# Kernel optimization log

Measured on AMD Instinct MI355X. Metric: run time of the kernel, lower is better.

The kernel has to match this reference:

```python
import jax, jax.numpy as jnp
import numpy as np

B, S, D, H, DK, DFF, L = 4, 1024, 1024, 16, 64, 4096, 128

def setup_inputs() -> dict:
    key = jax.random.key(0)
    ks = jax.random.split(key, 20)
    stdv = 1.0 / np.sqrt(D)
    u = lambda k, shape, s=stdv: jax.random.uniform(k, shape, jnp.float32, -s, s)
    x = jax.random.normal(ks[0], (B, S, D), jnp.float32)
    causal = jnp.triu(jnp.ones((S, S), bool), 1)          # True = masked
    attn_mask = jnp.broadcast_to(causal, (B, S, S))
    return {
        "x": x,
        "attn_mask": attn_mask,
        "W_q": u(ks[1], (H * DK, D)), "b_q": jnp.zeros((H * DK,)),
        "W_k": u(ks[2], (H * DK, D)), "b_k": jnp.zeros((H * DK,)),
        "W_v": u(ks[3], (H * DK, D)), "b_v": jnp.zeros((H * DK,)),
        "W_o": u(ks[4], (D, H * DK)), "b_o": jnp.zeros((D,)),
        "W_rel": u(ks[5], (2 * L + 1, DK), 1.0 / np.sqrt(DK)),
        "ln1_alpha": jnp.ones((D,)), "ln1_bias": jnp.zeros((D,)),
        "ln2_alpha": jnp.ones((D,)), "ln2_bias": jnp.zeros((D,)),
        "W1": u(ks[6], (DFF, D)), "b1": jnp.zeros((DFF,)),
        "W2": u(ks[7], (D, DFF)), "b2": jnp.zeros((D,)),
    }

def _layer_norm(x, alpha, bias, eps=1e-5):
    # Faithful to source: (x - mean) / (std + eps), std is biased (unbiased=False)
    m = jnp.mean(x, axis=-1, keepdims=True)
    std = jnp.sqrt(jnp.mean((x - m) ** 2, axis=-1, keepdims=True))
    return alpha * (x - m) / (std + eps) + bias

def reference(x, attn_mask, W_q, b_q, W_k, b_k, W_v, b_v, W_o, b_o, W_rel,
              ln1_alpha, ln1_bias, ln2_alpha, ln2_bias, W1, b1, W2, b2):
    b, s, d = x.shape
    q = (x @ W_q.T + b_q).reshape(b, s, H, DK)
    k = (x @ W_k.T + b_k).reshape(b, s, H, DK)
    v = (x @ W_v.T + b_v).reshape(b, s, H, DK)
    # relative position bias table lookup -> [s, s, DK]
    idx = jnp.clip(jnp.arange(s)[:, None] - jnp.arange(s)[None, :], -L, L) + L
    pos = W_rel[idx]
    # NOTE: original uses rel_pos_k_emb for BOTH pos_key and pos_value (as in source).
    scores = jnp.einsum('bqnd,bknd->bnqk', q, k) + jnp.einsum('bqnd,qkd->bnqk', q, pos)
    scores = scores / np.sqrt(DK)
    scores = jnp.where(attn_mask[:, None, :, :], jnp.float32(-10000.0), scores)
    attn = jax.nn.softmax(scores, axis=-1)
    out = jnp.einsum('bnqk,bknd->bnqd', attn, v) + jnp.einsum('bnqk,qkd->bnqd', attn, pos)
    out = out.transpose(0, 2, 1, 3).reshape(b, s, H * DK)
    out = out @ W_o.T + b_o
    # post-LN transformer layer: LN(x + attn), then LN(h + FFN(h))
    h = _layer_norm(x + out, ln1_alpha, ln1_bias)
    f = jax.nn.relu(h @ W1.T + b1) @ W2.T + b2
    return _layer_norm(h + f, ln2_alpha, ln2_bias)
```

## Files before the change

kernel.cpp:

```cpp
#include <hip/hip_runtime.h>
#include <cmath>
#include <cstdint>

typedef __bf16 bf16;
typedef __bf16 bf16x8 __attribute__((ext_vector_type(8)));
typedef __bf16 bf16x4 __attribute__((ext_vector_type(4)));
typedef float f32x4 __attribute__((ext_vector_type(4)));

#define CEXP 0.1803368852f

__device__ __forceinline__ void async_ld16(const void* g, void* l) {
  __builtin_amdgcn_global_load_lds(
      (__attribute__((address_space(1))) void*)(uintptr_t)g,
      (__attribute__((address_space(3))) void*)l, 16, 0, 0);
}

__global__ __launch_bounds__(256) void cast_all(
    const float* __restrict__ x,  const float* __restrict__ wq, const float* __restrict__ wk,
    const float* __restrict__ wv, const float* __restrict__ wo, const float* __restrict__ w1,
    const float* __restrict__ w2,
    bf16* xb, bf16* wqb, bf16* wkb, bf16* wvb, bf16* wob, bf16* w1b, bf16* w2b)
{
  int i = blockIdx.x * 256 + threadIdx.x;
  const int M1 = 1 << 20, Q = 1 << 18;
  const float* src; bf16* dst; int off;
  if      (i < M1)            { src = x;  dst = xb;  off = i; }
  else if (i < M1 + Q)        { src = wq; dst = wqb; off = i - M1; }
  else if (i < M1 + 2 * Q)    { src = wk; dst = wkb; off = i - M1 - Q; }
  else if (i < M1 + 3 * Q)    { src = wv; dst = wvb; off = i - M1 - 2 * Q; }
  else if (i < M1 + 4 * Q)    { src = wo; dst = wob; off = i - M1 - 3 * Q; }
  else if (i < 3 * M1)        { src = w1; dst = w1b; off = i - M1 - 4 * Q; }
  else                        { src = w2; dst = w2b; off = i - 3 * M1; }
  float4 v = ((const float4*)src)[off];
  bf16x4 o; o[0]=(bf16)v.x; o[1]=(bf16)v.y; o[2]=(bf16)v.z; o[3]=(bf16)v.w;
  ((bf16x4*)dst)[off] = o;
}

template<int BM>
__device__ __forceinline__ void gemm_core(
    const bf16* __restrict__ A, const bf16* __restrict__ Bm, const float* __restrict__ bias,
    float* __restrict__ outF, bf16* __restrict__ outB,
    const float* __restrict__ residF, const bf16* __restrict__ residB,
    int N, int kld, int kbeg, int kend, int relu, bf16* As, bf16* Bs)
{
  constexpr int MI = BM / 32;
  const int tid  = threadIdx.x;
  const int wave = tid >> 6, lane = tid & 63;
  const int lr = lane & 15, lq = lane >> 4;
  const int bm = blockIdx.x * BM, bn = blockIdx.y * 128;
  const int wm = (wave >> 1) * (BM / 2), wn = (wave & 1) * 64;
  const int srow = lane >> 2, scol = (lane & 3) * 8;

  const f32x4 fz = {0.f, 0.f, 0.f, 0.f};
  f32x4 acc[MI][4];
#pragma unroll
  for (int i = 0; i < MI; i++)
#pragma unroll
    for (int j = 0; j < 4; j++) acc[i][j] = fz;

  auto issue = [&](int k0, int buf) {
    bf16* Ad = As + buf * (BM * 32);
    bf16* Bd = Bs + buf * (128 * 32);
    if (BM == 128) {
#pragma unroll
      for (int cc = 0; cc < 2; ++cc) {
        int c = wave * 2 + cc;
        async_ld16(A + (size_t)(bm + c * 16 + srow) * kld + k0 + scol, Ad + c * 512);
      }
    } else {
      async_ld16(A + (size_t)(bm + wave * 16 + srow) * kld + k0 + scol, Ad + wave * 512);
    }
#pragma unroll
    for (int cc = 0; cc < 2; ++cc) {
      int c = wave * 2 + cc;
      async_ld16(Bm + (size_t)(bn + c * 16 + srow) * kld + k0 + scol, Bd + c * 512);
    }
  };

  const int nit = (kend - kbeg) >> 5;
  issue(kbeg, 0);
  for (int i = 0; i < nit; i++) {
    __syncthreads();
    if (i + 1 < nit) issue(kbeg + (i + 1) * 32, (i + 1) & 1);
    const bf16* Ab = As + (i & 1) * (BM * 32);
    const bf16* Bb = Bs + (i & 1) * (128 * 32);
    bf16x8 af[MI], bfr[4];
#pragma unroll
    for (int mi = 0; mi < MI; mi++) af[mi]  = *(const bf16x8*)(Ab + (wm + mi*16 + lr)*32 + lq*8);
#pragma unroll
    for (int ni = 0; ni < 4; ni++) bfr[ni] = *(const bf16x8*)(Bb + (wn + ni*16 + lr)*32 + lq*8);
#pragma unroll
    for (int mi = 0; mi < MI; mi++)
#pragma unroll
      for (int ni = 0; ni < 4; ni++)
        acc[mi][ni] = __builtin_amdgcn_mfma_f32_16x16x32_bf16(af[mi], bfr[ni], acc[mi][ni], 0, 0, 0);
  }

#pragma unroll
  for (int ni = 0; ni < 4; ni++) {
    int n = bn + wn + ni*16 + lr;
    float bv = bias ? bias[n] : 0.0f;
#pragma unroll
    for (int mi = 0; mi < MI; mi++) {
#pragma unroll
      for (int r = 0; r < 4; r++) {
        int m = bm + wm + mi*16 + lq*4 + r;
        size_t idx = (size_t)m * N + n;
        float v = acc[mi][ni][r] + bv;
        if (relu) v = fmaxf(v, 0.0f);
        if (residF) v += residF[idx];
        if (residB) v += (float)residB[idx];
        if (outF) outF[idx] = v;
        else      outB[idx] = (bf16)v;
      }
    }
  }
}

template<int BM>
__global__ __launch_bounds__(256) void gemm_bt(
    const bf16* A, const bf16* Bm, const float* bias,
    float* outF, bf16* outB, const float* residF, const bf16* residB,
    int N, int K, int relu)
{
  __shared__ bf16 As[2 * BM * 32];
  __shared__ bf16 Bs[2 * 128 * 32];
  gemm_core<BM>(A, Bm, bias, outF, outB, residF, residB, N, K, 0, K, relu, As, Bs);
}

__global__ __launch_bounds__(256) void gemm_splitk(
    const bf16* A, const bf16* Bm, float* part, int N, int kld, int kchunk)
{
  __shared__ bf16 As[2 * 128 * 32];
  __shared__ bf16 Bs[2 * 128 * 32];
  const int z = blockIdx.z;
  gemm_core<128>(A, Bm, nullptr, part + (size_t)z * 4096 * N, nullptr, nullptr, nullptr,
                 N, kld, z * kchunk, (z + 1) * kchunk, 0, As, Bs);
}

__global__ __launch_bounds__(256) void gemm_qkv(
    const bf16* A, const bf16* Bq, const bf16* Bk, const bf16* Bv,
    const float* bq, const float* bk, const float* bv,
    bf16* Oq, bf16* Ok, bf16* Ov, int N, int K)
{
  __shared__ bf16 As[2 * 128 * 32];
  __shared__ bf16 Bs[2 * 128 * 32];
  const bf16* Bm  = blockIdx.z == 0 ? Bq : (blockIdx.z == 1 ? Bk : Bv);
  const float* bi = blockIdx.z == 0 ? bq : (blockIdx.z == 1 ? bk : bv);
  bf16* O         = blockIdx.z == 0 ? Oq : (blockIdx.z == 1 ? Ok : Ov);
  gemm_core<128>(A, Bm, bi, nullptr, O, nullptr, nullptr, N, K, 0, K, 0, As, Bs);
}

__global__ __launch_bounds__(256) void transpose_v(const bf16* __restrict__ V, bf16* __restrict__ Vt) {
  __shared__ bf16 t[64][72];
  const int tid = threadIdx.x;
  const int sblk = blockIdx.x;
  const int bh = blockIdx.y;
  const int b = bh >> 4, h = bh & 15;
  const int sr = tid >> 2, dc = (tid & 3) * 16;
  const bf16* src = V + ((size_t)(b * 1024 + sblk * 64 + sr)) * 1024 + h * 64 + dc;
  bf16x8 r0 = *(const bf16x8*)src;
  bf16x8 r1 = *(const bf16x8*)(src + 8);
  *(bf16x8*)(&t[sr][dc]) = r0;
  *(bf16x8*)(&t[sr][dc + 8]) = r1;
  __syncthreads();
  const int dr = tid >> 2, sc = (tid & 3) * 16;
  bf16 o[16];
#pragma unroll
  for (int j = 0; j < 16; j++) o[j] = t[sc + j][dr];
  bf16* dst = Vt + ((size_t)(bh * 64 + dr)) * 1024 + sblk * 64 + sc;
  *(bf16x8*)dst = *(bf16x8*)&o[0];
  *(bf16x8*)(dst + 8) = *(bf16x8*)&o[8];
}

#define S_LEN 1024
#define ROWSTR 1024

__global__ __launch_bounds__(256) void attn_kernel(
    const bf16* __restrict__ Qg, const bf16* __restrict__ Kg, const bf16* __restrict__ Vt,
    const float* __restrict__ Wrel, bf16* __restrict__ Og)
{
  __shared__ __align__(16) bf16 hist[64][136];
  __shared__ __align__(16) bf16 rel_s[64][132];
  __shared__ __align__(16) bf16 ovl[8704];
  bf16* V_T  = ovl;
  bf16* Pb   = ovl + 4096;
  bf16* Wst  = ovl;
  bf16* Wr_t = ovl;
  float* lbuf = (float*)rel_s;
  float* hbuf = lbuf + 256;

  const int tid = threadIdx.x;
  const int wave = tid >> 6, lane = tid & 63;
  const int lr = lane & 15, lq = lane >> 4;
  const int qblk = 15 - blockIdx.x;
  const int bh = blockIdx.y;
  const int b = bh >> 4, h = bh & 15;
  const int q0 = qblk * 64;
  const int T = qblk + 1;
  const int nearStart = (T > 3) ? T - 3 : 0;
  const size_t rowbase = (size_t)b * S_LEN * ROWSTR + h * 64;
  const size_t vtbase = (size_t)(bh * 64) * 1024;
  const f32x4 fz = {0.f, 0.f, 0.f, 0.f};

  for (int e = tid; e < 128 * 64; e += 256)
    Wst[e] = (bf16)Wrel[(size_t)(128 + (e >> 6)) * 64 + (e & 63)];
  for (int e = tid; e < 64 * 68; e += 256) ((uint*)hist)[e] = 0u;

  bf16x8 qf[4][2];
#pragma unroll
  for (int qt = 0; qt < 4; qt++)
#pragma unroll
    for (int c = 0; c < 2; c++)
      qf[qt][c] = *(const bf16x8*)(Qg + rowbase + (size_t)(q0 + qt*16 + lr) * ROWSTR + c*32 + lq*8);

  bf16x8 wb[2];
#pragma unroll
  for (int c = 0; c < 2; c++)
#pragma unroll
    for (int j = 0; j < 8; j++)
      wb[c][j] = (bf16)Wrel[(size_t)256 * 64 + c*32 + lq*8 + j];

  __syncthreads();

#pragma unroll
  for (int tt = 0; tt < 2; ++tt)
#pragma unroll
    for (int qt = 0; qt < 4; ++qt) {
      f32x4 a = fz;
#pragma unroll
      for (int c = 0; c < 2; c++) {
        bf16x8 wf = *(const bf16x8*)(Wst + (wave*32 + tt*16 + lr) * 64 + c*32 + lq*8);
        a = __builtin_amdgcn_mfma_f32_16x16x32_bf16(wf, qf[qt][c], a, 0, 0, 0);
      }
      bf16x4 pk; pk[0]=(bf16)(a[0]*CEXP); pk[1]=(bf16)(a[1]*CEXP);
                 pk[2]=(bf16)(a[2]*CEXP); pk[3]=(bf16)(a[3]*CEXP);
      *(bf16x4*)(&rel_s[qt*16 + lr][wave*32 + tt*16 + lq*4]) = pk;
    }
  {
    f32x4 a = fz;
#pragma unroll
    for (int c = 0; c < 2; c++)
      a = __builtin_amdgcn_mfma_f32_16x16x32_bf16(wb[c], qf[wave][c], a, 0, 0, 0);
    if (lq == 0) rel_s[wave*16 + lr][128] = (bf16)(a[0]*CEXP);
  }
  __syncthreads();

  float relc[4];
#pragma unroll
  for (int qt = 0; qt < 4; qt++) relc[qt] = (float)rel_s[qt*16 + lr][128];

  float l_p[4] = {0.f,0.f,0.f,0.f}, h_p[4] = {0.f,0.f,0.f,0.f};
  f32x4 acc_o[4];
#pragma unroll
  for (int dt = 0; dt < 4; dt++) acc_o[dt] = fz;

  const int vd1 = tid >> 3;
  const int vj  = (tid & 7) ^ (vd1 & 7);
  const int krow = 16 * wave + lr;

  uint4 va, vb, va2, vb2;
  bf16x8 kf0, kf1, kn0, kn1;
  {
    const bf16* vp = Vt + vtbase + (size_t)vd1 * 1024 + vj * 8;
    va = *(const uint4*)vp; vb = *(const uint4*)(vp + 32 * 1024);
    const bf16* kp = Kg + rowbase + (size_t)krow * ROWSTR + lq*8;
    kf0 = *(const bf16x8*)kp; kf1 = *(const bf16x8*)(kp + 32);
  }

  for (int kt = 0; kt < T; ++kt) {
    const int k0 = kt * 64;

    f32x4 sc[4];
#pragma unroll
    for (int qt = 0; qt < 4; qt++) {
      sc[qt] = __builtin_amdgcn_mfma_f32_16x16x32_bf16(kf0, qf[qt][0], fz, 0, 0, 0);
      sc[qt] = __builtin_amdgcn_mfma_f32_16x16x32_bf16(kf1, qf[qt][1], sc[qt], 0, 0, 0);
    }
    if (kt + 1 < T) {
      const bf16* vp = Vt + vtbase + (size_t)vd1 * 1024 + k0 + 64 + vj * 8;
      va2 = *(const uint4*)vp; vb2 = *(const uint4*)(vp + 32 * 1024);
      const bf16* kp = Kg + rowbase + (size_t)(k0 + 64 + krow) * ROWSTR + lq*8;
      kn0 = *(const bf16x8*)kp; kn1 = *(const bf16x8*)(kp + 32);
    }

    float pw[4][4];
    if (kt < nearStart) {
#pragma unroll
      for (int qt = 0; qt < 4; qt++) {
#pragma unroll
        for (int r = 0; r < 4; r++) pw[qt][r] = exp2f(fmaf(sc[qt][r], CEXP, relc[qt]));
        float s4 = pw[qt][0] + pw[qt][1] + pw[qt][2] + pw[qt][3];
        l_p[qt] += s4; h_p[qt] += s4;
      }
    } else {
#pragma unroll
      for (int qt = 0; qt < 4; qt++) {
        int qg = q0 + qt*16 + lr;
#pragma unroll
        for (int r = 0; r < 4; r++) {
          int kg = k0 + 16*wave + lq*4 + r;
          float p = 0.0f;
          if (kg <= qg) {
            int t = qg - kg; int tc = t > 128 ? 128 : t;
            p = exp2f(fmaf(sc[qt][r], CEXP, (float)rel_s[qt*16 + lr][tc]));
            l_p[qt] += p;
            if (t >= 128) h_p[qt] += p;
            else          hist[qt*16 + lr][t] = (bf16)p;
          }
          pw[qt][r] = p;
        }
      }
    }

    __syncthreads();
    *(uint4*)(V_T + tid * 8) = va;
    *(uint4*)(V_T + (tid + 256) * 8) = vb;
#pragma unroll
    for (int qt = 0; qt < 4; qt++) {
      bf16x4 pk; pk[0]=(bf16)pw[qt][0]; pk[1]=(bf16)pw[qt][1];
                 pk[2]=(bf16)pw[qt][2]; pk[3]=(bf16)pw[qt][3];
      *(bf16x4*)(Pb + (qt*16 + lr) * 72 + 16*wave + lq*4) = pk;
    }
    __syncthreads();

#pragma unroll
    for (int c = 0; c < 2; c++) {
      bf16x8 pf = *(const bf16x8*)(Pb + (16*wave + lr) * 72 + c*32 + lq*8);
#pragma unroll
      for (int dt = 0; dt < 4; dt++) {
        int vd = dt*16 + lr;
        int jx = (c*4 + lq) ^ (vd & 7);
        bf16x8 vf = *(const bf16x8*)(V_T + ((vd << 3) + jx) * 8);
        acc_o[dt] = __builtin_amdgcn_mfma_f32_16x16x32_bf16(pf, vf, acc_o[dt], 0, 0, 0);
      }
    }
    kf0 = kn0; kf1 = kn1; va = va2; vb = vb2;
  }

#pragma unroll
  for (int qt = 0; qt < 4; qt++) {
    l_p[qt] += __shfl_xor(l_p[qt], 16); l_p[qt] += __shfl_xor(l_p[qt], 32);
    h_p[qt] += __shfl_xor(h_p[qt], 16); h_p[qt] += __shfl_xor(h_p[qt], 32);
  }
  __syncthreads();
  if (lq == 0) {
#pragma unroll
    for (int qt = 0; qt < 4; qt++) {
      lbuf[wave*64 + qt*16 + lr] = l_p[qt];
      hbuf[wave*64 + qt*16 + lr] = h_p[qt];
    }
  }
  for (int e = tid; e < 64 * 128; e += 256) {
    int d = e >> 7, t = e & 127;
    Wr_t[d * 136 + t] = (bf16)Wrel[(size_t)(128 + t) * 64 + d];
  }
  __syncthreads();
#pragma unroll
  for (int c = 0; c < 4; c++) {
    bf16x8 hf = *(const bf16x8*)&hist[wave*16 + lr][c*32 + lq*8];
#pragma unroll
    for (int dt = 0; dt < 4; dt++) {
      bf16x8 wf = *(const bf16x8*)(Wr_t + (dt*16 + lr) * 136 + c*32 + lq*8);
      acc_o[dt] = __builtin_amdgcn_mfma_f32_16x16x32_bf16(hf, wf, acc_o[dt], 0, 0, 0);
    }
  }
  float l4[4], h4[4];
#pragma unroll
  for (int r = 0; r < 4; r++) {
    int q = wave*16 + lq*4 + r;
    l4[r] = lbuf[q] + lbuf[64+q] + lbuf[128+q] + lbuf[192+q];
    h4[r] = hbuf[q] + hbuf[64+q] + hbuf[128+q] + hbuf[192+q];
  }
#pragma unroll
  for (int dt = 0; dt < 4; dt++) {
    float wv = Wrel[(size_t)256 * 64 + dt*16 + lr];
#pragma unroll
    for (int r = 0; r < 4; r++) acc_o[dt][r] += h4[r] * wv;
  }
#pragma unroll
  for (int dt = 0; dt < 4; dt++)
#pragma unroll
    for (int r = 0; r < 4; r++) {
      int qg = q0 + wave*16 + lq*4 + r;
      Og[rowbase + (size_t)qg * ROWSTR + dt*16 + lr] = (bf16)(acc_o[dt][r] / l4[r]);
    }
}

__global__ __launch_bounds__(256) void ln_fuse(
    const float* __restrict__ pA, const float* __restrict__ pB,
    const float* __restrict__ bias,
    const float* __restrict__ residF, const bf16* __restrict__ residB,
    const float* __restrict__ alpha, const float* __restrict__ beta,
    float* __restrict__ outF, bf16* __restrict__ outB)
{
  const int row = blockIdx.x, tid = threadIdx.x;
  const int lane = tid & 63, wave = tid >> 6;
  const size_t base = (size_t)row * 1024;
  float4 v = ((const float4*)(pA + base))[tid];
  float4 v2 = ((const float4*)(pB + base))[tid];
  v.x += v2.x; v.y += v2.y; v.z += v2.z; v.w += v2.w;
  float4 bv = ((const float4*)bias)[tid];
  v.x += bv.x; v.y += bv.y; v.z += bv.z; v.w += bv.w;
  if (residF) {
    float4 rv = ((const float4*)(residF + base))[tid];
    v.x += rv.x; v.y += rv.y; v.z += rv.z; v.w += rv.w;
  }
  if (residB) {
    bf16x4 rv = ((const bf16x4*)(residB + base))[tid];
    v.x += (float)rv[0]; v.y += (float)rv[1]; v.z += (float)rv[2]; v.w += (float)rv[3];
  }
  float s  = v.x + v.y + v.z + v.w;
  float ss = v.x*v.x + v.y*v.y + v.z*v.z + v.w*v.w;
#pragma unroll
  for (int off = 32; off; off >>= 1) { s += __shfl_down(s, off); ss += __shfl_down(ss, off); }
  __shared__ float rs[4], rss[4];
  if (lane == 0) { rs[wave] = s; rss[wave] = ss; }
  __syncthreads();
  s  = rs[0] + rs[1] + rs[2] + rs[3];
  ss = rss[0] + rss[1] + rss[2] + rss[3];
  float mean = s * (1.0f / 1024.0f);
  float var  = ss * (1.0f / 1024.0f) - mean * mean;
  float inv  = 1.0f / (sqrtf(fmaxf(var, 0.0f)) + 1e-5f);
  float4 a = ((const float4*)alpha)[tid];
  float4 bb = ((const float4*)beta)[tid];
  float o0 = a.x * (v.x - mean) * inv + bb.x;
  float o1 = a.y * (v.y - mean) * inv + bb.y;
  float o2 = a.z * (v.z - mean) * inv + bb.z;
  float o3 = a.w * (v.w - mean) * inv + bb.w;
  if (outF) { float4 o = {o0, o1, o2, o3}; ((float4*)(outF + base))[tid] = o; }
  if (outB) { bf16x4 o; o[0]=(bf16)o0; o[1]=(bf16)o1; o[2]=(bf16)o2; o[3]=(bf16)o3;
              ((bf16x4*)(outB + base))[tid] = o; }
}

extern "C" void kernel_launch(void* const* d_in, const int* in_sizes, int n_in,
                              void* d_out, int out_size, void* d_ws, size_t ws_size,
                              hipStream_t stream) {
  (void)in_sizes; (void)n_in; (void)out_size; (void)ws_size;
  const int D = 1024, DFF = 4096;

  const float* x    = (const float*)d_in[0];
  const float* Wq   = (const float*)d_in[2];
  const float* bq   = (const float*)d_in[3];
  const float* Wk   = (const float*)d_in[4];
  const float* bk   = (const float*)d_in[5];
  const float* Wv   = (const float*)d_in[6];
  const float* bv   = (const float*)d_in[7];
  const float* Wo   = (const float*)d_in[8];
  const float* bo   = (const float*)d_in[9];
  const float* Wrel = (const float*)d_in[10];
  const float* g1   = (const float*)d_in[11];
  const float* be1  = (const float*)d_in[12];
  const float* g2   = (const float*)d_in[13];
  const float* be2  = (const float*)d_in[14];
  const float* W1   = (const float*)d_in[15];
  const float* b1   = (const float*)d_in[16];
  const float* W2   = (const float*)d_in[17];
  const float* b2   = (const float*)d_in[18];

  char* ws = (char*)d_ws;
  const size_t MB = 1024 * 1024;
  bf16*  xb   = (bf16*)(ws + 0);
  bf16*  Wqb  = (bf16*)(ws + 8  * MB);
  bf16*  Wkb  = (bf16*)(ws + 10 * MB);
  bf16*  Wvb  = (bf16*)(ws + 12 * MB);
  bf16*  Wob  = (bf16*)(ws + 14 * MB);
  bf16*  W1b  = (bf16*)(ws + 16 * MB);
  bf16*  W2b  = (bf16*)(ws + 24 * MB);
  bf16*  Qb   = (bf16*)(ws + 32 * MB);
  bf16*  Kb   = (bf16*)(ws + 40 * MB);
  bf16*  Vb   = (bf16*)(ws + 48 * MB);
  bf16*  Vt   = (bf16*)(ws + 56 * MB);
  bf16*  AOb  = (bf16*)(ws + 48 * MB);
  float* part = (float*)(ws + 64 * MB);
  bf16*  f1   = Qb;
  bf16*  hb   = xb;

  cast_all<<<16384, 256, 0, stream>>>(x, Wq, Wk, Wv, Wo, W1, W2,
                                      xb, Wqb, Wkb, Wvb, Wob, W1b, W2b);

  gemm_qkv<<<dim3(32, 8, 3), 256, 0, stream>>>(xb, Wqb, Wkb, Wvb, bq, bk, bv, Qb, Kb, Vb, D, D);
  transpose_v<<<dim3(16, 64), 256, 0, stream>>>(Vb, Vt);
  attn_kernel<<<dim3(16, 64), 256, 0, stream>>>(Qb, Kb, Vt, Wrel, AOb);
  gemm_splitk<<<dim3(32, 8, 2), 256, 0, stream>>>(AOb, Wob, part, D, D, 512);
  ln_fuse<<<4096, 256, 0, stream>>>(part, part + 4096 * 1024, bo, x, nullptr, g1, be1, nullptr, hb);
  gemm_bt<128><<<dim3(32, 32), 256, 0, stream>>>(hb, W1b, b1, nullptr, f1, nullptr, nullptr, DFF, D, 1);
  gemm_splitk<<<dim3(32, 8, 2), 256, 0, stream>>>(f1, W2b, part, D, DFF, 2048);
  ln_fuse<<<4096, 256, 0, stream>>>(part, part + 4096 * 1024, b2, nullptr, hb, g2, be2, (float*)d_out, nullptr);
}
```

Before: 413.7 us.

## Fuse V transpose into QKV GEMM, restructure PV in attention, bf16 split-K partials

The QKV GEMM epilogue now writes V directly in transposed per-head layout, which removes the separate transpose kernel. The attention kernel builds the P·V MFMA operands from registers by pairing two key tiles, so the per-tile LDS staging and its two barriers go away. Per-wave partial outputs are then reduced through shared-memory atomics. Split-K partials are stored as bf16 instead of fp32, and the FFN down-projection uses a 4-way split, which cuts partial-buffer traffic at some cost in accumulation precision.

```diff
diff --git a/kernel.cpp b/kernel.cpp
--- a/kernel.cpp
+++ b/kernel.cpp
@@ -41,7 +41,7 @@
     const bf16* __restrict__ A, const bf16* __restrict__ Bm, const float* __restrict__ bias,
     float* __restrict__ outF, bf16* __restrict__ outB,
     const float* __restrict__ residF, const bf16* __restrict__ residB,
-    int N, int kld, int kbeg, int kend, int relu, bf16* As, bf16* Bs)
+    int N, int kld, int kbeg, int kend, int relu, int vtrans, bf16* As, bf16* Bs)
 {
   constexpr int MI = BM / 32;
   const int tid  = threadIdx.x;
@@ -96,6 +96,24 @@
         acc[mi][ni] = __builtin_amdgcn_mfma_f32_16x16x32_bf16(af[mi], bfr[ni], acc[mi][ni], 0, 0, 0);
   }
 
+  if (vtrans) {
+#pragma unroll
+    for (int ni = 0; ni < 4; ni++) {
+      int n = bn + wn + ni*16 + lr;
+      float bv = bias ? bias[n] : 0.0f;
+      int hh = n >> 6, dd = n & 63;
+#pragma unroll
+      for (int mi = 0; mi < MI; mi++) {
+        int m0 = bm + wm + mi*16 + lq*4;
+        int bb = m0 >> 10, s = m0 & 1023;
+        bf16x4 o;
+#pragma unroll
+        for (int r = 0; r < 4; r++) o[r] = (bf16)(acc[mi][ni][r] + bv);
+        *(bf16x4*)(outB + ((size_t)((bb * 16 + hh) * 64 + dd)) * 1024 + s) = o;
+      }
+    }
+    return;
+  }
 #pragma unroll
   for (int ni = 0; ni < 4; ni++) {
     int n = bn + wn + ni*16 + lr;
@@ -125,52 +143,31 @@
 {
   __shared__ bf16 As[2 * BM * 32];
   __shared__ bf16 Bs[2 * 128 * 32];
-  gemm_core<BM>(A, Bm, bias, outF, outB, residF, residB, N, K, 0, K, relu, As, Bs);
+  gemm_core<BM>(A, Bm, bias, outF, outB, residF, residB, N, K, 0, K, relu, 0, As, Bs);
 }
 
 __global__ __launch_bounds__(256) void gemm_splitk(
-    const bf16* A, const bf16* Bm, float* part, int N, int kld, int kchunk)
+    const bf16* A, const bf16* Bm, bf16* part, int N, int kld, int kchunk)
 {
   __shared__ bf16 As[2 * 128 * 32];
   __shared__ bf16 Bs[2 * 128 * 32];
   const int z = blockIdx.z;
-  gemm_core<128>(A, Bm, nullptr, part + (size_t)z * 4096 * N, nullptr, nullptr, nullptr,
-                 N, kld, z * kchunk, (z + 1) * kchunk, 0, As, Bs);
+  gemm_core<128>(A, Bm, nullptr, nullptr, part + (size_t)z * 4194304, nullptr, nullptr,
+                 N, kld, z * kchunk, (z + 1) * kchunk, 0, 0, As, Bs);
 }
 
 __global__ __launch_bounds__(256) void gemm_qkv(
     const bf16* A, const bf16* Bq, const bf16* Bk, const bf16* Bv,
     const float* bq, const float* bk, const float* bv,
-    bf16* Oq, bf16* Ok, bf16* Ov, int N, int K)
+    bf16* Oq, bf16* Ok, bf16* Ovt, int N, int K)
 {
   __shared__ bf16 As[2 * 128 * 32];
   __shared__ bf16 Bs[2 * 128 * 32];
-  const bf16* Bm  = blockIdx.z == 0 ? Bq : (blockIdx.z == 1 ? Bk : Bv);
-  const float* bi = blockIdx.z == 0 ? bq : (blockIdx.z == 1 ? bk : bv);
-  bf16* O         = blockIdx.z == 0 ? Oq : (blockIdx.z == 1 ? Ok : Ov);
-  gemm_core<128>(A, Bm, bi, nullptr, O, nullptr, nullptr, N, K, 0, K, 0, As, Bs);
-}
-
-__global__ __launch_bounds__(256) void transpose_v(const bf16* __restrict__ V, bf16* __restrict__ Vt) {
-  __shared__ bf16 t[64][72];
-  const int tid = threadIdx.x;
-  const int sblk = blockIdx.x;
-  const int bh = blockIdx.y;
-  const int b = bh >> 4, h = bh & 15;
-  const int sr = tid >> 2, dc = (tid & 3) * 16;
-  const bf16* src = V + ((size_t)(b * 1024 + sblk * 64 + sr)) * 1024 + h * 64 + dc;
-  bf16x8 r0 = *(const bf16x8*)src;
-  bf16x8 r1 = *(const bf16x8*)(src + 8);
-  *(bf16x8*)(&t[sr][dc]) = r0;
-  *(bf16x8*)(&t[sr][dc + 8]) = r1;
-  __syncthreads();
-  const int dr = tid >> 2, sc = (tid & 3) * 16;
-  bf16 o[16];
-#pragma unroll
-  for (int j = 0; j < 16; j++) o[j] = t[sc + j][dr];
-  bf16* dst = Vt + ((size_t)(bh * 64 + dr)) * 1024 + sblk * 64 + sc;
-  *(bf16x8*)dst = *(bf16x8*)&o[0];
-  *(bf16x8*)(dst + 8) = *(bf16x8*)&o[8];
+  const int z = blockIdx.z;
+  const bf16* Bm  = z == 0 ? Bq : (z == 1 ? Bk : Bv);
+  const float* bi = z == 0 ? bq : (z == 1 ? bk : bv);
+  bf16* O         = z == 0 ? Oq : (z == 1 ? Ok : Ovt);
+  gemm_core<128>(A, Bm, bi, nullptr, O, nullptr, nullptr, N, K, 0, K, 0, (z == 2), As, Bs);
 }
 
 #define S_LEN 1024
@@ -181,14 +178,10 @@
     const float* __restrict__ Wrel, bf16* __restrict__ Og)
 {
   __shared__ __align__(16) bf16 hist[64][136];
-  __shared__ __align__(16) bf16 rel_s[64][132];
-  __shared__ __align__(16) bf16 ovl[8704];
-  bf16* V_T  = ovl;
-  bf16* Pb   = ovl + 4096;
-  bf16* Wst  = ovl;
-  bf16* Wr_t = ovl;
-  float* lbuf = (float*)rel_s;
-  float* hbuf = lbuf + 256;
+  __shared__ __align__(16) bf16 rel_s[64][136];
+  __shared__ __align__(16) float Obuf[64][64];
+  __shared__ float lbuf[256];
+  __shared__ float hbuf[256];
 
   const int tid = threadIdx.x;
   const int wave = tid >> 6, lane = tid & 63;
@@ -200,9 +193,10 @@
   const int T = qblk + 1;
   const int nearStart = (T > 3) ? T - 3 : 0;
   const size_t rowbase = (size_t)b * S_LEN * ROWSTR + h * 64;
-  const size_t vtbase = (size_t)(bh * 64) * 1024;
+  const size_t vtbase = (size_t)bh * 65536;
   const f32x4 fz = {0.f, 0.f, 0.f, 0.f};
 
+  bf16* Wst = (bf16*)Obuf;
   for (int e = tid; e < 128 * 64; e += 256)
     Wst[e] = (bf16)Wrel[(size_t)(128 + (e >> 6)) * 64 + (e & 63)];
   for (int e = tid; e < 64 * 68; e += 256) ((uint*)hist)[e] = 0u;
@@ -249,24 +243,26 @@
   float relc[4];
 #pragma unroll
   for (int qt = 0; qt < 4; qt++) relc[qt] = (float)rel_s[qt*16 + lr][128];
+  for (int e = tid; e < 4096; e += 256) ((float*)Obuf)[e] = 0.0f;
+  __syncthreads();
 
   float l_p[4] = {0.f,0.f,0.f,0.f}, h_p[4] = {0.f,0.f,0.f,0.f};
-  f32x4 acc_o[4];
-#pragma unroll
-  for (int dt = 0; dt < 4; dt++) acc_o[dt] = fz;
-
-  const int vd1 = tid >> 3;
-  const int vj  = (tid & 7) ^ (vd1 & 7);
-  const int krow = 16 * wave + lr;
-
-  uint4 va, vb, va2, vb2;
+  f32x4 acc[4][4];
+#pragma unroll
+  for (int qt = 0; qt < 4; qt++)
+#pragma unroll
+    for (int dt = 0; dt < 4; dt++) acc[qt][dt] = fz;
+
+  const int krow = 16*wave + lr;
+  const int kcol = 16*wave + lq*4;
   bf16x8 kf0, kf1, kn0, kn1;
   {
-    const bf16* vp = Vt + vtbase + (size_t)vd1 * 1024 + vj * 8;
-    va = *(const uint4*)vp; vb = *(const uint4*)(vp + 32 * 1024);
     const bf16* kp = Kg + rowbase + (size_t)krow * ROWSTR + lq*8;
     kf0 = *(const bf16x8*)kp; kf1 = *(const bf16x8*)(kp + 32);
   }
+
+  bf16x4 pfb[4], vfb[4];
+  int phase = 0;
 
   for (int kt = 0; kt < T; ++kt) {
     const int k0 = kt * 64;
@@ -277,21 +273,26 @@
       sc[qt] = __builtin_amdgcn_mfma_f32_16x16x32_bf16(kf0, qf[qt][0], fz, 0, 0, 0);
       sc[qt] = __builtin_amdgcn_mfma_f32_16x16x32_bf16(kf1, qf[qt][1], sc[qt], 0, 0, 0);
     }
+    bf16x4 vf[4];
+#pragma unroll
+    for (int dt = 0; dt < 4; dt++)
+      vf[dt] = *(const bf16x4*)(Vt + vtbase + (size_t)(dt*16 + lr) * 1024 + k0 + kcol);
     if (kt + 1 < T) {
-      const bf16* vp = Vt + vtbase + (size_t)vd1 * 1024 + k0 + 64 + vj * 8;
-      va2 = *(const uint4*)vp; vb2 = *(const uint4*)(vp + 32 * 1024);
       const bf16* kp = Kg + rowbase + (size_t)(k0 + 64 + krow) * ROWSTR + lq*8;
       kn0 = *(const bf16x8*)kp; kn1 = *(const bf16x8*)(kp + 32);
     }
 
-    float pw[4][4];
+    bf16x4 pf[4];
     if (kt < nearStart) {
 #pragma unroll
       for (int qt = 0; qt < 4; qt++) {
-#pragma unroll
-        for (int r = 0; r < 4; r++) pw[qt][r] = exp2f(fmaf(sc[qt][r], CEXP, relc[qt]));
-        float s4 = pw[qt][0] + pw[qt][1] + pw[qt][2] + pw[qt][3];
+        float p0 = exp2f(fmaf(sc[qt][0], CEXP, relc[qt]));
+        float p1 = exp2f(fmaf(sc[qt][1], CEXP, relc[qt]));
+        float p2 = exp2f(fmaf(sc[qt][2], CEXP, relc[qt]));
+        float p3 = exp2f(fmaf(sc[qt][3], CEXP, relc[qt]));
+        float s4 = p0 + p1 + p2 + p3;
         l_p[qt] += s4; h_p[qt] += s4;
+        pf[qt][0]=(bf16)p0; pf[qt][1]=(bf16)p1; pf[qt][2]=(bf16)p2; pf[qt][3]=(bf16)p3;
       }
     } else {
 #pragma unroll
@@ -308,34 +309,43 @@
             if (t >= 128) h_p[qt] += p;
             else          hist[qt*16 + lr][t] = (bf16)p;
           }
-          pw[qt][r] = p;
+          pf[qt][r] = (bf16)p;
         }
       }
     }
 
-    __syncthreads();
-    *(uint4*)(V_T + tid * 8) = va;
-    *(uint4*)(V_T + (tid + 256) * 8) = vb;
+    if (phase == 0) {
+#pragma unroll
+      for (int qt = 0; qt < 4; qt++) pfb[qt] = pf[qt];
+#pragma unroll
+      for (int dt = 0; dt < 4; dt++) vfb[dt] = vf[dt];
+      phase = 1;
+    } else {
+#pragma unroll
+      for (int qt = 0; qt < 4; qt++) {
+        bf16x8 p8 = __builtin_shufflevector(pfb[qt], pf[qt], 0,1,2,3,4,5,6,7);
+#pragma unroll
+        for (int dt = 0; dt < 4; dt++) {
+          bf16x8 v8 = __builtin_shufflevector(vfb[dt], vf[dt], 0,1,2,3,4,5,6,7);
+          acc[qt][dt] = __builtin_amdgcn_mfma_f32_16x16x32_bf16(p8, v8, acc[qt][dt], 0, 0, 0);
+        }
+      }
+      phase = 0;
+    }
+
+    kf0 = kn0; kf1 = kn1;
+  }
+  if (phase) {
+    const bf16x4 z4 = {};
 #pragma unroll
     for (int qt = 0; qt < 4; qt++) {
-      bf16x4 pk; pk[0]=(bf16)pw[qt][0]; pk[1]=(bf16)pw[qt][1];
-                 pk[2]=(bf16)pw[qt][2]; pk[3]=(bf16)pw[qt][3];
-      *(bf16x4*)(Pb + (qt*16 + lr) * 72 + 16*wave + lq*4) = pk;
-    }
-    __syncthreads();
-
-#pragma unroll
-    for (int c = 0; c < 2; c++) {
-      bf16x8 pf = *(const bf16x8*)(Pb + (16*wave + lr) * 72 + c*32 + lq*8);
+      bf16x8 p8 = __builtin_shufflevector(pfb[qt], z4, 0,1,2,3,4,5,6,7);
 #pragma unroll
       for (int dt = 0; dt < 4; dt++) {
-        int vd = dt*16 + lr;
-        int jx = (c*4 + lq) ^ (vd & 7);
-        bf16x8 vf = *(const bf16x8*)(V_T + ((vd << 3) + jx) * 8);
-        acc_o[dt] = __builtin_amdgcn_mfma_f32_16x16x32_bf16(pf, vf, acc_o[dt], 0, 0, 0);
-      }
-    }
-    kf0 = kn0; kf1 = kn1; va = va2; vb = vb2;
+        bf16x8 v8 = __builtin_shufflevector(vfb[dt], z4, 0,1,2,3,4,5,6,7);
+        acc[qt][dt] = __builtin_amdgcn_mfma_f32_16x16x32_bf16(p8, v8, acc[qt][dt], 0, 0, 0);
+      }
+    }
   }
 
 #pragma unroll
@@ -344,6 +354,14 @@
     h_p[qt] += __shfl_xor(h_p[qt], 16); h_p[qt] += __shfl_xor(h_p[qt], 32);
   }
   __syncthreads();
+
+#pragma unroll
+  for (int qt = 0; qt < 4; qt++)
+#pragma unroll
+    for (int dt = 0; dt < 4; dt++)
+#pragma unroll
+      for (int r = 0; r < 4; r++)
+        atomicAdd(&Obuf[qt*16 + lq*4 + r][dt*16 + lr], acc[qt][dt][r]);
   if (lq == 0) {
 #pragma unroll
     for (int qt = 0; qt < 4; qt++) {
@@ -351,11 +369,20 @@
       hbuf[wave*64 + qt*16 + lr] = h_p[qt];
     }
   }
+  bf16* Wr_t = &rel_s[0][0];
   for (int e = tid; e < 64 * 128; e += 256) {
     int d = e >> 7, t = e & 127;
     Wr_t[d * 136 + t] = (bf16)Wrel[(size_t)(128 + t) * 64 + d];
   }
   __syncthreads();
+
+  f32x4 acc_o[4];
+#pragma unroll
+  for (int dt = 0; dt < 4; dt++)
+#pragma unroll
+    for (int r = 0; r < 4; r++)
+      acc_o[dt][r] = Obuf[wave*16 + lq*4 + r][dt*16 + lr];
+
 #pragma unroll
   for (int c = 0; c < 4; c++) {
     bf16x8 hf = *(const bf16x8*)&hist[wave*16 + lr][c*32 + lq*8];
@@ -387,8 +414,8 @@
     }
 }
 
-__global__ __launch_bounds__(256) void ln_fuse(
-    const float* __restrict__ pA, const float* __restrict__ pB,
+__global__ __launch_bounds__(256) void ln_fuseB(
+    const bf16* __restrict__ parts, int np,
     const float* __restrict__ bias,
     const float* __restrict__ residF, const bf16* __restrict__ residB,
     const float* __restrict__ alpha, const float* __restrict__ beta,
@@ -396,18 +423,20 @@
 {
   const int row = blockIdx.x, tid = threadIdx.x;
   const int lane = tid & 63, wave = tid >> 6;
-  const size_t base = (size_t)row * 1024;
-  float4 v = ((const float4*)(pA + base))[tid];
-  float4 v2 = ((const float4*)(pB + base))[tid];
-  v.x += v2.x; v.y += v2.y; v.z += v2.z; v.w += v2.w;
+  const size_t base = (size_t)row * 1024 + tid * 4;
+  float4 v = {0.f, 0.f, 0.f, 0.f};
+  for (int p = 0; p < np; p++) {
+    bf16x4 pv = *(const bf16x4*)(parts + (size_t)p * 4194304 + base);
+    v.x += (float)pv[0]; v.y += (float)pv[1]; v.z += (float)pv[2]; v.w += (float)pv[3];
+  }
   float4 bv = ((const float4*)bias)[tid];
   v.x += bv.x; v.y += bv.y; v.z += bv.z; v.w += bv.w;
   if (residF) {
-    float4 rv = ((const float4*)(residF + base))[tid];
+    float4 rv = *(const float4*)(residF + base);
     v.x += rv.x; v.y += rv.y; v.z += rv.z; v.w += rv.w;
   }
   if (residB) {
-    bf16x4 rv = ((const bf16x4*)(residB + base))[tid];
+    bf16x4 rv = *(const bf16x4*)(residB + base);
     v.x += (float)rv[0]; v.y += (float)rv[1]; v.z += (float)rv[2]; v.w += (float)rv[3];
   }
   float s  = v.x + v.y + v.z + v.w;
@@ -428,9 +457,9 @@
   float o1 = a.y * (v.y - mean) * inv + bb.y;
   float o2 = a.z * (v.z - mean) * inv + bb.z;
   float o3 = a.w * (v.w - mean) * inv + bb.w;
-  if (outF) { float4 o = {o0, o1, o2, o3}; ((float4*)(outF + base))[tid] = o; }
+  if (outF) { float4 o = {o0, o1, o2, o3}; *(float4*)(outF + base) = o; }
   if (outB) { bf16x4 o; o[0]=(bf16)o0; o[1]=(bf16)o1; o[2]=(bf16)o2; o[3]=(bf16)o3;
-              ((bf16x4*)(outB + base))[tid] = o; }
+              *(bf16x4*)(outB + base) = o; }
 }
 
 extern "C" void kernel_launch(void* const* d_in, const int* in_sizes, int n_in,
@@ -469,22 +498,20 @@
   bf16*  W2b  = (bf16*)(ws + 24 * MB);
   bf16*  Qb   = (bf16*)(ws + 32 * MB);
   bf16*  Kb   = (bf16*)(ws + 40 * MB);
-  bf16*  Vb   = (bf16*)(ws + 48 * MB);
-  bf16*  Vt   = (bf16*)(ws + 56 * MB);
-  bf16*  AOb  = (bf16*)(ws + 48 * MB);
-  float* part = (float*)(ws + 64 * MB);
+  bf16*  Vt   = (bf16*)(ws + 48 * MB);
+  bf16*  AOb  = (bf16*)(ws + 56 * MB);
+  bf16*  partb= (bf16*)(ws + 64 * MB);
   bf16*  f1   = Qb;
   bf16*  hb   = xb;
 
   cast_all<<<16384, 256, 0, stream>>>(x, Wq, Wk, Wv, Wo, W1, W2,
                                       xb, Wqb, Wkb, Wvb, Wob, W1b, W2b);
 
-  gemm_qkv<<<dim3(32, 8, 3), 256, 0, stream>>>(xb, Wqb, Wkb, Wvb, bq, bk, bv, Qb, Kb, Vb, D, D);
-  transpose_v<<<dim3(16, 64), 256, 0, stream>>>(Vb, Vt);
+  gemm_qkv<<<dim3(32, 8, 3), 256, 0, stream>>>(xb, Wqb, Wkb, Wvb, bq, bk, bv, Qb, Kb, Vt, D, D);
   attn_kernel<<<dim3(16, 64), 256, 0, stream>>>(Qb, Kb, Vt, Wrel, AOb);
-  gemm_splitk<<<dim3(32, 8, 2), 256, 0, stream>>>(AOb, Wob, part, D, D, 512);
-  ln_fuse<<<4096, 256, 0, stream>>>(part, part + 4096 * 1024, bo, x, nullptr, g1, be1, nullptr, hb);
+  gemm_splitk<<<dim3(32, 8, 2), 256, 0, stream>>>(AOb, Wob, partb, D, D, 512);
+  ln_fuseB<<<4096, 256, 0, stream>>>(partb, 2, bo, x, nullptr, g1, be1, nullptr, hb);
   gemm_bt<128><<<dim3(32, 32), 256, 0, stream>>>(hb, W1b, b1, nullptr, f1, nullptr, nullptr, DFF, D, 1);
-  gemm_splitk<<<dim3(32, 8, 2), 256, 0, stream>>>(f1, W2b, part, D, DFF, 2048);
-  ln_fuse<<<4096, 256, 0, stream>>>(part, part + 4096 * 1024, b2, nullptr, hb, g2, be2, (float*)d_out, nullptr);
-}
+  gemm_splitk<<<dim3(32, 8, 4), 256, 0, stream>>>(f1, W2b, partb, D, DFF, 1024);
+  ln_fuseB<<<4096, 256, 0, stream>>>(partb, 4, b2, nullptr, hb, g2, be2, (float*)d_out, nullptr);
+}
```

Result: slower. 504.6 us (+22.0%).
